# Performance work log

Measured on AMD Instinct MI355X. Metric: run time of the kernel, lower is better.

## Reference

```python
import jax, jax.numpy as jnp
import numpy as np

N_HEAD_HALF = 8          # config.n_head // 2
LAMBDA_INIT = 0.2        # diff_lambda_init
RMS_EPS = 1.1920929e-07  # torch.finfo(float32).eps (F.rms_norm default)
ROPE_BASE = 10000.0


def setup_inputs() -> dict:
    key = jax.random.key(0)
    ks = jax.random.split(key, 9)
    B, T, C = 2, 2048, 2048
    HD = C // N_HEAD_HALF  # 256
    s = 0.02
    return {
        "x": jax.random.normal(ks[0], (B, T, C), jnp.float32),
        "wq": jax.random.normal(ks[1], (C, C), jnp.float32) * s,
        "wk": jax.random.normal(ks[2], (C, C), jnp.float32) * s,
        "wv": jax.random.normal(ks[3], (C, C), jnp.float32) * s,
        "wo": jax.random.normal(ks[4], (C, C), jnp.float32) * s,
        "lq1": jax.random.normal(ks[5], (HD,), jnp.float32) * 0.1,
        "lk1": jax.random.normal(ks[6], (HD,), jnp.float32) * 0.1,
        "lq2": jax.random.normal(ks[7], (HD,), jnp.float32) * 0.1,
        "lk2": jax.random.normal(ks[8], (HD,), jnp.float32) * 0.1,
    }


def _rms_norm(x):
    var = jnp.mean(x * x, axis=-1, keepdims=True)
    return x * jax.lax.rsqrt(var + RMS_EPS)


def _rotary(x):
    # Faithful to original bug: positions run along axis 1 (the HEAD axis),
    # since Rotary is applied after transpose(1,2). x: (B, NH, T, D)
    d = x.shape[-1]
    inv_freq = (1.0 / ROPE_BASE) ** (jnp.arange(0, d, 2, dtype=jnp.float32) / d)
    t = jnp.arange(x.shape[1], dtype=jnp.float32)
    freqs = jnp.outer(t, inv_freq)                      # (NH, d/2)
    cos = jnp.cos(freqs)[None, :, None, :]
    sin = jnp.sin(freqs)[None, :, None, :]
    x1, x2 = jnp.split(x, 2, axis=-1)
    return jnp.concatenate((x1 * cos + x2 * sin, -x1 * sin + x2 * cos), axis=-1)


def _causal_attn(q, k, v, scale):
    # q,k: (B,NH,T,Dh)  v: (B,NH,T,HD)
    T = q.shape[2]
    s = jnp.einsum("bhqd,bhkd->bhqk", q, k) * scale
    mask = jnp.tril(jnp.ones((T, T), dtype=bool))
    s = jnp.where(mask, s, jnp.float32(-jnp.inf))
    p = jax.nn.softmax(s, axis=-1)
    return jnp.einsum("bhqk,bhkd->bhqd", p, v)


def reference(x, wq, wk, wv, wo, lq1, lk1, lq2, lk2):
    B, T, C = x.shape
    NH = N_HEAD_HALF
    HD = C // NH
    HH = HD // 2

    lam1 = jnp.exp(jnp.sum(lq1 * lk1))
    lam2 = jnp.exp(jnp.sum(lq2 * lk2))
    lam = lam1 - lam2 + LAMBDA_INIT

    q = (x @ wq.T).reshape(B, T, NH, 2, HH).transpose(0, 2, 1, 3, 4)
    k = (x @ wk.T).reshape(B, T, NH, 2, HH).transpose(0, 2, 1, 3, 4)
    v = (x @ wv.T).reshape(B, T, NH, HD).transpose(0, 2, 1, 3)

    q1 = _rotary(_rms_norm(q[..., 0, :]))
    q2 = _rotary(_rms_norm(q[..., 1, :]))
    k1 = _rotary(_rms_norm(k[..., 0, :]))
    k2 = _rotary(_rms_norm(k[..., 1, :]))

    scale = 1.0 / jnp.sqrt(jnp.float32(HH))
    y = _causal_attn(q1, k1, v, scale) - lam * _causal_attn(q2, k2, v, scale)

    y = y.transpose(0, 2, 1, 3).reshape(B, T, C)
    y = (y @ wo.T) * (1.0 - LAMBDA_INIT)
    return y
```

## Files before the change

kernel.cpp:

```cpp
#include <hip/hip_runtime.h>
#include <hip/hip_bf16.h>

using bf16 = __hip_bfloat16;
typedef __bf16 bf16x8_t __attribute__((ext_vector_type(8)));
typedef __bf16 bf16x4_t __attribute__((ext_vector_type(4)));
typedef float f32x4  __attribute__((ext_vector_type(4)));
typedef float f32x16 __attribute__((ext_vector_type(16)));

#define AS1 __attribute__((address_space(1)))
#define AS3 __attribute__((address_space(3)))

__device__ __forceinline__ void gll16(const void* g, void* l) {
  __builtin_amdgcn_global_load_lds((const AS1 void*)g, (AS3 void*)l, 16u, 0, 0u);
}

__device__ __forceinline__ __bf16 tobf(float f) {
  bf16 h = __float2bfloat16(f);
  return __builtin_bit_cast(__bf16, h);
}

__global__ __launch_bounds__(256) void k_cvt(
    const float* __restrict__ x,  const float* __restrict__ wq,
    const float* __restrict__ wk, const float* __restrict__ wv,
    const float* __restrict__ wo,
    bf16* __restrict__ xb,  bf16* __restrict__ wqb, bf16* __restrict__ wkb,
    bf16* __restrict__ wvb, bf16* __restrict__ wob) {
  size_t id = (size_t)blockIdx.x * 256 + threadIdx.x;
  const float* s; bf16* d; size_t off;
  if (id < 2097152) { s = x; d = xb; off = id; }
  else {
    size_t r = id - 2097152;
    unsigned w = (unsigned)(r >> 20);
    off = r & 1048575u;
    s = (w == 0) ? wq : (w == 1) ? wk : (w == 2) ? wv : wo;
    d = (w == 0) ? wqb : (w == 1) ? wkb : (w == 2) ? wvb : wob;
  }
  const float4 v = ((const float4*)s)[off];
  bf16x4_t o = { tobf(v.x), tobf(v.y), tobf(v.z), tobf(v.w) };
  *(bf16x4_t*)(d + off * 4) = o;
}

__global__ __launch_bounds__(256) void k_lam(
    const float* __restrict__ lq1, const float* __restrict__ lk1,
    const float* __restrict__ lq2, const float* __restrict__ lk2,
    float* __restrict__ lam) {
  __shared__ float r1[4], r2[4];
  int t = threadIdx.x;
  float a = lq1[t] * lk1[t];
  float b = lq2[t] * lk2[t];
#pragma unroll
  for (int s = 1; s < 64; s <<= 1) { a += __shfl_xor(a, s); b += __shfl_xor(b, s); }
  if ((t & 63) == 0) { r1[t >> 6] = a; r2[t >> 6] = b; }
  __syncthreads();
  if (t == 0) {
    float s1 = r1[0] + r1[1] + r1[2] + r1[3];
    float s2 = r2[0] + r2[1] + r2[2] + r2[3];
    *lam = expf(s1) - expf(s2) + 0.2f;
  }
}

__device__ __forceinline__ void gemm_core(
    const bf16* __restrict__ A, const bf16* __restrict__ Bm,
    int m0, int n0, bf16* lA, bf16* lB, f32x4 (&acc)[4][4]) {
  const int tid  = threadIdx.x;
  const int lane = tid & 63;
  const int g    = lane >> 4;
  const int l15  = lane & 15;
  const int l7   = lane & 7;
  const int wave = tid >> 6;
  const int wm   = (wave >> 1) * 64;
  const int wn   = (wave & 1) * 64;

  int srow[4], ssc[4];
#pragma unroll
  for (int j = 0; j < 4; ++j) {
    int id = tid + j * 256;
    srow[j] = id >> 3;
    ssc[j]  = (id & 7) ^ (srow[j] & 7);
  }

  for (int k0 = 0; k0 < 2048; k0 += 64) {
    __syncthreads();
#pragma unroll
    for (int j = 0; j < 4; ++j) {
      int id = tid + j * 256;
      gll16(A  + (size_t)(m0 + srow[j]) * 2048 + k0 + ssc[j] * 8, lA + id * 8);
      gll16(Bm + (size_t)(n0 + srow[j]) * 2048 + k0 + ssc[j] * 8, lB + id * 8);
    }
    __syncthreads();
#pragma unroll
    for (int ks = 0; ks < 2; ++ks) {
      const int pc = (ks * 4 + g) ^ l7;
      bf16x8_t af[4], bfr[4];
#pragma unroll
      for (int mt = 0; mt < 4; ++mt)
        af[mt] = *(const bf16x8_t*)(lA + (wm + mt * 16 + l15) * 64 + pc * 8);
#pragma unroll
      for (int nt = 0; nt < 4; ++nt)
        bfr[nt] = *(const bf16x8_t*)(lB + (wn + nt * 16 + l15) * 64 + pc * 8);
#pragma unroll
      for (int mt = 0; mt < 4; ++mt)
#pragma unroll
        for (int nt = 0; nt < 4; ++nt)
          acc[mt][nt] = __builtin_amdgcn_mfma_f32_16x16x32_bf16(
              af[mt], bfr[nt], acc[mt][nt], 0, 0, 0);
    }
  }
}

__global__ __launch_bounds__(256) void k_gemm_qkv(
    const bf16* __restrict__ xb,
    const bf16* __restrict__ wqb, const bf16* __restrict__ wkb,
    const bf16* __restrict__ wvb,
    bf16* __restrict__ Qb, bf16* __restrict__ Kb, bf16* __restrict__ vt) {
  __shared__ __align__(16) bf16 lA[128 * 64];
  __shared__ __align__(16) bf16 lB[128 * 64];
  const int z  = blockIdx.z;
  const bf16* Bm = (z == 0) ? wqb : (z == 1) ? wkb : wvb;
  const int m0 = blockIdx.y * 128, n0 = blockIdx.x * 128;
  f32x4 acc[4][4] = {};
  gemm_core(xb, Bm, m0, n0, lA, lB, acc);

  const int lane = threadIdx.x & 63, wave = threadIdx.x >> 6;
  const int g = lane >> 4, l15 = lane & 15;
  const int wm = (wave >> 1) * 64, wn = (wave & 1) * 64;
  if (z < 2) {
    bf16* Out = z ? Kb : Qb;
#pragma unroll
    for (int mt = 0; mt < 4; ++mt)
#pragma unroll
      for (int nt = 0; nt < 4; ++nt) {
        int row = m0 + wm + mt * 16 + 4 * g;
        int col = n0 + wn + nt * 16 + l15;
#pragma unroll
        for (int r = 0; r < 4; ++r)
          Out[(size_t)(row + r) * 2048 + col] = __float2bfloat16(acc[mt][nt][r]);
      }
  } else {
#pragma unroll
    for (int mt = 0; mt < 4; ++mt)
#pragma unroll
      for (int nt = 0; nt < 4; ++nt) {
        int rb  = m0 + wm + mt * 16 + 4 * g;
        int col = n0 + wn + nt * 16 + l15;
        int nh = col >> 8, hd = col & 255;
        int b = rb >> 11, t = rb & 2047;
        bf16x4_t pv;
#pragma unroll
        for (int r = 0; r < 4; ++r) pv[r] = tobf(acc[mt][nt][r]);
        *(bf16x4_t*)(vt + ((size_t)((b * 8 + nh) * 256 + hd)) * 2048 + t) = pv;
      }
  }
}

__global__ __launch_bounds__(256) void k_gemm_out(
    const bf16* __restrict__ yb, const bf16* __restrict__ wob,
    float* __restrict__ outp) {
  __shared__ __align__(16) bf16 lA[128 * 64];
  __shared__ __align__(16) bf16 lB[128 * 64];
  const int m0 = blockIdx.y * 128, n0 = blockIdx.x * 128;
  f32x4 acc[4][4] = {};
  gemm_core(yb, wob, m0, n0, lA, lB, acc);
  const int lane = threadIdx.x & 63, wave = threadIdx.x >> 6;
  const int g = lane >> 4, l15 = lane & 15;
  const int wm = (wave >> 1) * 64, wn = (wave & 1) * 64;
#pragma unroll
  for (int mt = 0; mt < 4; ++mt)
#pragma unroll
    for (int nt = 0; nt < 4; ++nt) {
      int row = m0 + wm + mt * 16 + 4 * g;
      int col = n0 + wn + nt * 16 + l15;
#pragma unroll
      for (int r = 0; r < 4; ++r)
        outp[(size_t)(row + r) * 2048 + col] = acc[mt][nt][r] * 0.8f;
    }
}

__global__ __launch_bounds__(256) void k_rmsrot(
    const bf16* __restrict__ Qb, const bf16* __restrict__ Kb,
    bf16* __restrict__ q1, bf16* __restrict__ q2,
    bf16* __restrict__ k1, bf16* __restrict__ k2) {
  const int lane = threadIdx.x & 63, wave = threadIdx.x >> 6;
  const int task = blockIdx.x * 4 + wave;
  const int which = task & 1;
  const int p  = (task >> 1) & 1;
  const int nh = (task >> 2) & 7;
  const int tok = task >> 5;
  const bf16* src = (which ? Kb : Qb) + (size_t)tok * 2048 + nh * 256 + p * 128;
  float x1 = __bfloat162float(src[lane]);
  float x2 = __bfloat162float(src[lane + 64]);
  float ss = x1 * x1 + x2 * x2;
#pragma unroll
  for (int s = 1; s < 64; s <<= 1) ss += __shfl_xor(ss, s);
  float inv = rsqrtf(ss * (1.0f / 128.0f) + 1.1920929e-07f);
  float n1 = x1 * inv, n2 = x2 * inv;
  float fr = exp2f(-(float)lane * 0.20762050593045951f);
  float ang = (float)nh * fr;
  float sn, cs;
  sincosf(ang, &sn, &cs);
  float o1 = n1 * cs + n2 * sn;
  float o2 = n2 * cs - n1 * sn;
  bf16* dst = (which ? (p ? k2 : k1) : (p ? q2 : q1)) + ((size_t)tok * 8 + nh) * 128;
  dst[lane]      = __float2bfloat16(o1);
  dst[lane + 64] = __float2bfloat16(o2);
}

__global__ __launch_bounds__(256, 1) void k_flash(
    const bf16* __restrict__ q1b, const bf16* __restrict__ q2b,
    const bf16* __restrict__ k1b, const bf16* __restrict__ k2b,
    const bf16* __restrict__ vtb, const float* __restrict__ lamp,
    bf16* __restrict__ yb) {
  __shared__ __align__(16) bf16 smem[65536];
  const int tid  = threadIdx.x;
  const int lane = tid & 63, wave = tid >> 6;
  const int pair = blockIdx.x;
  const int bh = blockIdx.y;
  const int b = bh >> 3, nh = bh & 7;
  const int at = wave & 1, qg = wave >> 1;
  const int l31 = lane & 31, g5 = lane >> 5, l7 = lane & 7;
  const float scale = 0.08838834764831845f;
  const float lam = *lamp;

  auto stage = [&](int kt, int buf) {
    bf16* dst = smem + buf * 32768;
    const int k0 = kt * 64;
#pragma unroll
    for (int it = 0; it < 4; ++it) {
      int id = tid + it * 256;
      int row = id >> 4, c = id & 15;
      int sc = (c & 8) | ((c & 7) ^ (row & 7));
      size_t goff = ((size_t)(b * 2048 + k0 + row) * 8 + nh) * 128 + sc * 8;
      gll16(k1b + goff, dst + id * 8);
      gll16(k2b + goff, dst + 8192 + id * 8);
    }
#pragma unroll
    for (int it = 0; it < 8; ++it) {
      int id = tid + it * 256;
      int row = id >> 3, c = id & 7;
      int sc = c ^ (row & 7);
      gll16(vtb + ((size_t)(bh * 256 + row)) * 2048 + k0 + sc * 8,
            dst + 16384 + id * 8);
    }
  };

  bf16x8_t qf[8];
  auto loadQ = [&](int qt) {
    int qglob = qt * 64 + qg * 32 + l31;
    const bf16* qp = (at ? q2b : q1b) +
                     ((size_t)(b * 2048 + qglob) * 8 + nh) * 128 + g5 * 8;
#pragma unroll
    for (int ks = 0; ks < 8; ++ks) qf[ks] = *(const bf16x8_t*)(qp + ks * 16);
  };

  f32x16 O[8];
  float mrun, lrun;
  auto resetO = [&]() {
#pragma unroll
    for (int i = 0; i < 8; ++i)
#pragma unroll
      for (int j = 0; j < 16; ++j) O[i][j] = 0.f;
    mrun = -1e30f; lrun = 0.f;
  };

  auto step = [&](int kt, int buf, int qt) {
    const bf16* lk = smem + buf * 32768 + (at ? 8192 : 0);
    const bf16* lv = smem + buf * 32768 + 16384;
    const int k0 = kt * 64;
    const int qglob = qt * 64 + qg * 32 + l31;

    f32x16 s0, s1;
#pragma unroll
    for (int j = 0; j < 16; ++j) { s0[j] = 0.f; s1[j] = 0.f; }
#pragma unroll
    for (int ks = 0; ks < 8; ++ks) {
      int cl = ks * 2 + g5;
      int pc = (cl & 8) | ((cl & 7) ^ l7);
      bf16x8_t a0 = *(const bf16x8_t*)(lk + l31 * 128 + pc * 8);
      bf16x8_t a1 = *(const bf16x8_t*)(lk + (32 + l31) * 128 + pc * 8);
      s0 = __builtin_amdgcn_mfma_f32_32x32x16_bf16(a0, qf[ks], s0, 0, 0, 0);
      s1 = __builtin_amdgcn_mfma_f32_32x32x16_bf16(a1, qf[ks], s1, 0, 0, 0);
    }

    const bool diag = (kt == qt);
    float rmax = -3.0e38f;
#pragma unroll
    for (int r = 0; r < 16; ++r) {
      int key0 = k0 + (r & 3) + 8 * (r >> 2) + 4 * g5;
      float v0 = s0[r] * scale;
      float v1 = s1[r] * scale;
      if (diag) {
        if (key0 > qglob)      v0 = -1e30f;
        if (key0 + 32 > qglob) v1 = -1e30f;
      }
      s0[r] = v0; s1[r] = v1;
      rmax = fmaxf(rmax, fmaxf(v0, v1));
    }
    rmax = fmaxf(rmax, __shfl_xor(rmax, 32));
    float mnew = fmaxf(mrun, rmax);
    float alpha = __expf(mrun - mnew);
    float psum = 0.f;
#pragma unroll
    for (int r = 0; r < 16; ++r) {
      float p0 = __expf(s0[r] - mnew);
      float p1 = __expf(s1[r] - mnew);
      s0[r] = p0; s1[r] = p1;
      psum += p0 + p1;
    }
    psum += __shfl_xor(psum, 32);
    lrun = lrun * alpha + psum;
    mrun = mnew;
#pragma unroll
    for (int i = 0; i < 8; ++i) O[i] *= alpha;

#pragma unroll
    for (int sl = 0; sl < 4; ++sl) {
      const int h = sl & 1;
      bf16x4_t lo, hi;
#pragma unroll
      for (int j = 0; j < 4; ++j) {
        float vl = (sl < 2) ? s0[h * 8 + j]     : s1[h * 8 + j];
        float vh = (sl < 2) ? s0[h * 8 + 4 + j] : s1[h * 8 + 4 + j];
        lo[j] = tobf(vl); hi[j] = tobf(vh);
      }
      bf16x4_t send = g5 ? lo : hi;
      int2 si = __builtin_bit_cast(int2, send);
      int2 ri;
      ri.x = __shfl_xor(si.x, 32);
      ri.y = __shfl_xor(si.y, 32);
      bf16x4_t recv = __builtin_bit_cast(bf16x4_t, ri);
      bf16x4_t f0 = g5 ? recv : lo;
      bf16x4_t f1 = g5 ? hi : recv;
      bf16x8_t pf = { f0[0], f0[1], f0[2], f0[3], f1[0], f1[1], f1[2], f1[3] };

      const int cl = sl * 2 + g5;
#pragma unroll
      for (int mt = 0; mt < 8; ++mt) {
        bf16x8_t vf = *(const bf16x8_t*)(lv + (mt * 32 + l31) * 64 + (cl ^ l7) * 8);
        O[mt] = __builtin_amdgcn_mfma_f32_32x32x16_bf16(vf, pf, O[mt], 0, 0, 0);
      }
    }
  };

  auto finish = [&](int qt, bf16* cb) {
    const int qglob = qt * 64 + qg * 32 + l31;
    const float invl = 1.f / lrun;
    __syncthreads();
    if (at) {
      const float f = lam * invl;
#pragma unroll
      for (int mt = 0; mt < 8; ++mt)
#pragma unroll
        for (int rq = 0; rq < 4; ++rq) {
          int hd = mt * 32 + 8 * rq + 4 * g5;
          bf16x4_t pv;
#pragma unroll
          for (int i = 0; i < 4; ++i) pv[i] = tobf(O[mt][rq * 4 + i] * f);
          *(bf16x4_t*)(cb + (size_t)(qg * 32 + l31) * 264 + hd) = pv;
        }
    }
    __syncthreads();
    if (!at) {
#pragma unroll
      for (int mt = 0; mt < 8; ++mt)
#pragma unroll
        for (int rq = 0; rq < 4; ++rq) {
          int hd = mt * 32 + 8 * rq + 4 * g5;
          bf16x4_t o2 = *(const bf16x4_t*)(cb + (size_t)(qg * 32 + l31) * 264 + hd);
          bf16x4_t pv;
#pragma unroll
          for (int i = 0; i < 4; ++i)
            pv[i] = tobf(O[mt][rq * 4 + i] * invl - (float)o2[i]);
          *(bf16x4_t*)(yb + (size_t)(b * 2048 + qglob) * 2048 + nh * 256 + hd) = pv;
        }
    }
  };

  const int qtB = 31 - pair, qtA = pair;

  loadQ(qtB);
  resetO();
  stage(0, 0);
  for (int kt = 0; kt <= qtB; ++kt) {
    __syncthreads();
    if (kt < qtB) stage(kt + 1, (kt + 1) & 1);
    else          stage(0, (kt + 1) & 1);
    step(kt, kt & 1, qtB);
  }
  finish(qtB, smem + (qtB & 1) * 32768);

  loadQ(qtA);
  resetO();
  for (int kt = 0; kt <= qtA; ++kt) {
    __syncthreads();
    if (kt < qtA) stage(kt + 1, (qtB + kt + 2) & 1);
    step(kt, (qtB + 1 + kt) & 1, qtA);
  }
  finish(qtA, smem + 32768);
}

extern "C" void kernel_launch(void* const* d_in, const int* in_sizes, int n_in,
                              void* d_out, int out_size, void* d_ws, size_t ws_size,
                              hipStream_t stream) {
  (void)in_sizes; (void)n_in; (void)out_size; (void)ws_size;
  const float* x   = (const float*)d_in[0];
  const float* wq  = (const float*)d_in[1];
  const float* wk  = (const float*)d_in[2];
  const float* wv  = (const float*)d_in[3];
  const float* wo  = (const float*)d_in[4];
  const float* lq1 = (const float*)d_in[5];
  const float* lk1 = (const float*)d_in[6];
  const float* lq2 = (const float*)d_in[7];
  const float* lk2 = (const float*)d_in[8];
  float* out = (float*)d_out;

  char* p = (char*)d_ws;
  float* lam = (float*)p;            p += 256;
  bf16* xb  = (bf16*)p;              p += (size_t)4096 * 2048 * 2;
  bf16* wqb = (bf16*)p;              p += (size_t)2048 * 2048 * 2;
  bf16* wkb = (bf16*)p;              p += (size_t)2048 * 2048 * 2;
  bf16* wvb = (bf16*)p;              p += (size_t)2048 * 2048 * 2;
  bf16* wob = (bf16*)p;              p += (size_t)2048 * 2048 * 2;
  bf16* Qb  = (bf16*)p;              p += (size_t)4096 * 2048 * 2;
  bf16* Kb  = (bf16*)p;              p += (size_t)4096 * 2048 * 2;
  bf16* vt  = (bf16*)p;              p += (size_t)4096 * 2048 * 2;
  bf16* q1b = (bf16*)p;              p += (size_t)4096 * 1024 * 2;
  bf16* q2b = (bf16*)p;              p += (size_t)4096 * 1024 * 2;
  bf16* k1b = (bf16*)p;              p += (size_t)4096 * 1024 * 2;
  bf16* k2b = (bf16*)p;              p += (size_t)4096 * 1024 * 2;
  bf16* yb  = (bf16*)p;              p += (size_t)4096 * 2048 * 2;

  k_cvt<<<24576, 256, 0, stream>>>(x, wq, wk, wv, wo, xb, wqb, wkb, wvb, wob);
  k_lam<<<1, 256, 0, stream>>>(lq1, lk1, lq2, lk2, lam);
  k_gemm_qkv<<<dim3(16, 32, 3), 256, 0, stream>>>(xb, wqb, wkb, wvb, Qb, Kb, vt);
  k_rmsrot<<<32768, 256, 0, stream>>>(Qb, Kb, q1b, q2b, k1b, k2b);
  k_flash<<<dim3(16, 16), 256, 0, stream>>>(q1b, q2b, k1b, k2b, vt, lam, yb);
  k_gemm_out<<<dim3(16, 32), 256, 0, stream>>>(yb, wob, out);
}
```

Measured before the change: 461.2 us.

## Fuse RMS-norm and rotary into QKV GEMM epilogue; vectorize output stores

The Q/K GEMM blocks now give each wave a full 128-column half-head, so RMS-norm and rotary can be applied in the epilogue. This removes the separate rmsrot kernel and the round trip of bf16 Q/K through global memory. The output GEMM swaps its MFMA operands so each lane holds contiguous columns, which allows 16-byte float4 stores. The changed wave tiling (2x8 per wave instead of 4x4) alters LDS read reuse and register pressure. Normalizing the fp32 accumulator directly also slightly changes rounding.

After: 431.2 us. 1.07x faster.

```diff
diff --git a/kernel.cpp b/kernel.cpp
--- a/kernel.cpp
+++ b/kernel.cpp
@@ -59,6 +59,7 @@
   }
 }
 
+template<bool SWAP>
 __device__ __forceinline__ void gemm_core(
     const bf16* __restrict__ A, const bf16* __restrict__ Bm,
     int m0, int n0, bf16* lA, bf16* lB, f32x4 (&acc)[4][4]) {
@@ -101,9 +102,14 @@
 #pragma unroll
       for (int mt = 0; mt < 4; ++mt)
 #pragma unroll
-        for (int nt = 0; nt < 4; ++nt)
-          acc[mt][nt] = __builtin_amdgcn_mfma_f32_16x16x32_bf16(
-              af[mt], bfr[nt], acc[mt][nt], 0, 0, 0);
+        for (int nt = 0; nt < 4; ++nt) {
+          if (SWAP)
+            acc[mt][nt] = __builtin_amdgcn_mfma_f32_16x16x32_bf16(
+                bfr[nt], af[mt], acc[mt][nt], 0, 0, 0);
+          else
+            acc[mt][nt] = __builtin_amdgcn_mfma_f32_16x16x32_bf16(
+                af[mt], bfr[nt], acc[mt][nt], 0, 0, 0);
+        }
     }
   }
 }
@@ -112,31 +118,99 @@
     const bf16* __restrict__ xb,
     const bf16* __restrict__ wqb, const bf16* __restrict__ wkb,
     const bf16* __restrict__ wvb,
-    bf16* __restrict__ Qb, bf16* __restrict__ Kb, bf16* __restrict__ vt) {
+    bf16* __restrict__ q1, bf16* __restrict__ q2,
+    bf16* __restrict__ k1, bf16* __restrict__ k2,
+    bf16* __restrict__ vt) {
   __shared__ __align__(16) bf16 lA[128 * 64];
   __shared__ __align__(16) bf16 lB[128 * 64];
+  __shared__ float lCs[64], lSn[64];
   const int z  = blockIdx.z;
-  const bf16* Bm = (z == 0) ? wqb : (z == 1) ? wkb : wvb;
   const int m0 = blockIdx.y * 128, n0 = blockIdx.x * 128;
-  f32x4 acc[4][4] = {};
-  gemm_core(xb, Bm, m0, n0, lA, lB, acc);
-
-  const int lane = threadIdx.x & 63, wave = threadIdx.x >> 6;
-  const int g = lane >> 4, l15 = lane & 15;
-  const int wm = (wave >> 1) * 64, wn = (wave & 1) * 64;
+  const int tid = threadIdx.x;
+  const int lane = tid & 63, wave = tid >> 6;
+  const int g = lane >> 4, l15 = lane & 15, l7 = lane & 7;
+
   if (z < 2) {
-    bf16* Out = z ? Kb : Qb;
-#pragma unroll
-    for (int mt = 0; mt < 4; ++mt)
-#pragma unroll
-      for (int nt = 0; nt < 4; ++nt) {
-        int row = m0 + wm + mt * 16 + 4 * g;
-        int col = n0 + wn + nt * 16 + l15;
-#pragma unroll
-        for (int r = 0; r < 4; ++r)
-          Out[(size_t)(row + r) * 2048 + col] = __float2bfloat16(acc[mt][nt][r]);
-      }
+    const bf16* Bm = z ? wkb : wqb;
+    f32x4 acc[2][8] = {};
+
+    int srow[4], ssc[4];
+#pragma unroll
+    for (int j = 0; j < 4; ++j) {
+      int id = tid + j * 256;
+      srow[j] = id >> 3;
+      ssc[j]  = (id & 7) ^ (srow[j] & 7);
+    }
+    for (int k0 = 0; k0 < 2048; k0 += 64) {
+      __syncthreads();
+#pragma unroll
+      for (int j = 0; j < 4; ++j) {
+        int id = tid + j * 256;
+        gll16(xb + (size_t)(m0 + srow[j]) * 2048 + k0 + ssc[j] * 8, lA + id * 8);
+        gll16(Bm + (size_t)(n0 + srow[j]) * 2048 + k0 + ssc[j] * 8, lB + id * 8);
+      }
+      __syncthreads();
+#pragma unroll
+      for (int ks = 0; ks < 2; ++ks) {
+        const int pc = (ks * 4 + g) ^ l7;
+        bf16x8_t af[2], bfr[8];
+#pragma unroll
+        for (int mt = 0; mt < 2; ++mt)
+          af[mt] = *(const bf16x8_t*)(lA + (wave * 32 + mt * 16 + l15) * 64 + pc * 8);
+#pragma unroll
+        for (int nt = 0; nt < 8; ++nt)
+          bfr[nt] = *(const bf16x8_t*)(lB + (nt * 16 + l15) * 64 + pc * 8);
+#pragma unroll
+        for (int mt = 0; mt < 2; ++mt)
+#pragma unroll
+          for (int nt = 0; nt < 8; ++nt)
+            acc[mt][nt] = __builtin_amdgcn_mfma_f32_16x16x32_bf16(
+                bfr[nt], af[mt], acc[mt][nt], 0, 0, 0);
+      }
+    }
+
+    const int nh = n0 >> 8, p = (n0 >> 7) & 1;
+    __syncthreads();
+    if (tid < 64) {
+      float fr = exp2f(-(float)tid * 0.20762050593045951f);
+      float sn, cs;
+      sincosf((float)nh * fr, &sn, &cs);
+      lCs[tid] = cs; lSn[tid] = sn;
+    }
+    __syncthreads();
+    bf16* dst = z ? (p ? k2 : k1) : (p ? q2 : q1);
+#pragma unroll
+    for (int mt = 0; mt < 2; ++mt) {
+      float ss = 0.f;
+#pragma unroll
+      for (int nt = 0; nt < 8; ++nt)
+#pragma unroll
+        for (int r = 0; r < 4; ++r) ss += acc[mt][nt][r] * acc[mt][nt][r];
+      ss += __shfl_xor(ss, 16);
+      ss += __shfl_xor(ss, 32);
+      const float inv = rsqrtf(ss * (1.0f / 128.0f) + 1.1920929e-07f);
+      const int tok = m0 + wave * 32 + mt * 16 + l15;
+      const size_t base = ((size_t)tok * 8 + nh) * 128;
+#pragma unroll
+      for (int nt4 = 0; nt4 < 4; ++nt4) {
+        const int jb = nt4 * 16 + 4 * g;
+        bf16x4_t o1v, o2v;
+#pragma unroll
+        for (int r = 0; r < 4; ++r) {
+          float cs = lCs[jb + r], sn = lSn[jb + r];
+          float x1 = acc[mt][nt4][r] * inv;
+          float x2 = acc[mt][nt4 + 4][r] * inv;
+          o1v[r] = tobf(x1 * cs + x2 * sn);
+          o2v[r] = tobf(x2 * cs - x1 * sn);
+        }
+        *(bf16x4_t*)(dst + base + jb)      = o1v;
+        *(bf16x4_t*)(dst + base + jb + 64) = o2v;
+      }
+    }
   } else {
+    f32x4 acc[4][4] = {};
+    gemm_core<false>(xb, wvb, m0, n0, lA, lB, acc);
+    const int wm = (wave >> 1) * 64, wn = (wave & 1) * 64;
 #pragma unroll
     for (int mt = 0; mt < 4; ++mt)
 #pragma unroll
@@ -160,7 +234,7 @@
   __shared__ __align__(16) bf16 lB[128 * 64];
   const int m0 = blockIdx.y * 128, n0 = blockIdx.x * 128;
   f32x4 acc[4][4] = {};
-  gemm_core(yb, wob, m0, n0, lA, lB, acc);
+  gemm_core<true>(yb, wob, m0, n0, lA, lB, acc);
   const int lane = threadIdx.x & 63, wave = threadIdx.x >> 6;
   const int g = lane >> 4, l15 = lane & 15;
   const int wm = (wave >> 1) * 64, wn = (wave & 1) * 64;
@@ -168,41 +242,13 @@
   for (int mt = 0; mt < 4; ++mt)
 #pragma unroll
     for (int nt = 0; nt < 4; ++nt) {
-      int row = m0 + wm + mt * 16 + 4 * g;
-      int col = n0 + wn + nt * 16 + l15;
-#pragma unroll
-      for (int r = 0; r < 4; ++r)
-        outp[(size_t)(row + r) * 2048 + col] = acc[mt][nt][r] * 0.8f;
-    }
-}
-
-__global__ __launch_bounds__(256) void k_rmsrot(
-    const bf16* __restrict__ Qb, const bf16* __restrict__ Kb,
-    bf16* __restrict__ q1, bf16* __restrict__ q2,
-    bf16* __restrict__ k1, bf16* __restrict__ k2) {
-  const int lane = threadIdx.x & 63, wave = threadIdx.x >> 6;
-  const int task = blockIdx.x * 4 + wave;
-  const int which = task & 1;
-  const int p  = (task >> 1) & 1;
-  const int nh = (task >> 2) & 7;
-  const int tok = task >> 5;
-  const bf16* src = (which ? Kb : Qb) + (size_t)tok * 2048 + nh * 256 + p * 128;
-  float x1 = __bfloat162float(src[lane]);
-  float x2 = __bfloat162float(src[lane + 64]);
-  float ss = x1 * x1 + x2 * x2;
-#pragma unroll
-  for (int s = 1; s < 64; s <<= 1) ss += __shfl_xor(ss, s);
-  float inv = rsqrtf(ss * (1.0f / 128.0f) + 1.1920929e-07f);
-  float n1 = x1 * inv, n2 = x2 * inv;
-  float fr = exp2f(-(float)lane * 0.20762050593045951f);
-  float ang = (float)nh * fr;
-  float sn, cs;
-  sincosf(ang, &sn, &cs);
-  float o1 = n1 * cs + n2 * sn;
-  float o2 = n2 * cs - n1 * sn;
-  bf16* dst = (which ? (p ? k2 : k1) : (p ? q2 : q1)) + ((size_t)tok * 8 + nh) * 128;
-  dst[lane]      = __float2bfloat16(o1);
-  dst[lane + 64] = __float2bfloat16(o2);
+      int row = m0 + wm + mt * 16 + l15;
+      int col = n0 + wn + nt * 16 + 4 * g;
+      f32x4 v;
+#pragma unroll
+      for (int r = 0; r < 4; ++r) v[r] = acc[mt][nt][r] * 0.8f;
+      *(f32x4*)(outp + (size_t)row * 2048 + col) = v;
+    }
 }
 
 __global__ __launch_bounds__(256, 1) void k_flash(
@@ -420,8 +466,6 @@
   bf16* wkb = (bf16*)p;              p += (size_t)2048 * 2048 * 2;
   bf16* wvb = (bf16*)p;              p += (size_t)2048 * 2048 * 2;
   bf16* wob = (bf16*)p;              p += (size_t)2048 * 2048 * 2;
-  bf16* Qb  = (bf16*)p;              p += (size_t)4096 * 2048 * 2;
-  bf16* Kb  = (bf16*)p;              p += (size_t)4096 * 2048 * 2;
   bf16* vt  = (bf16*)p;              p += (size_t)4096 * 2048 * 2;
   bf16* q1b = (bf16*)p;              p += (size_t)4096 * 1024 * 2;
   bf16* q2b = (bf16*)p;              p += (size_t)4096 * 1024 * 2;
@@ -431,8 +475,8 @@
 
   k_cvt<<<24576, 256, 0, stream>>>(x, wq, wk, wv, wo, xb, wqb, wkb, wvb, wob);
   k_lam<<<1, 256, 0, stream>>>(lq1, lk1, lq2, lk2, lam);
-  k_gemm_qkv<<<dim3(16, 32, 3), 256, 0, stream>>>(xb, wqb, wkb, wvb, Qb, Kb, vt);
-  k_rmsrot<<<32768, 256, 0, stream>>>(Qb, Kb, q1b, q2b, k1b, k2b);
+  k_gemm_qkv<<<dim3(16, 32, 3), 256, 0, stream>>>(xb, wqb, wkb, wvb,
+                                                  q1b, q2b, k1b, k2b, vt);
   k_flash<<<dim3(16, 16), 256, 0, stream>>>(q1b, q2b, k1b, k2b, vt, lam, yb);
   k_gemm_out<<<dim3(16, 32), 256, 0, stream>>>(yb, wob, out);
 }
```
